# Performance work log

Measured on AMD Instinct MI355X. Metric: run time of the kernel, lower is better.

## Reference

```python
import jax, jax.numpy as jnp
import numpy as np

B, T = 16, 40
NH, DEPTH, NCLASS, IMG_H, W_IMG = 128, 2, 6625, 32, 512
HIDDEN = 64  # nh < 256 -> hidden = 64
LINEAR_IN = NH * 8  # nh * int((32-3-1)/4+1)
BN_EPS = 1e-5


def _conv2d(x, w, b, stride, pad, groups=1):
    y = jax.lax.conv_general_dilated(
        x, w, (stride, stride), [(pad, pad), (pad, pad)],
        dimension_numbers=('NCHW', 'OIHW', 'NCHW'), feature_group_count=groups)
    return y + b[None, :, None, None]


def _conv_bn_act(x, w, b, g, bb, m, v, stride, pad, groups=1):
    y = _conv2d(x, w, b, stride, pad, groups)
    y = (y - m[None, :, None, None]) * jax.lax.rsqrt(v[None, :, None, None] + BN_EPS) \
        * g[None, :, None, None] + bb[None, :, None, None]
    return jax.nn.gelu(y, approximate=False)  # torch nn.GELU default = exact erf


def _gru(xs, wih, whh, bih, bhh):
    # torch GRU gate order: r, z, n. xs: [B, T, D] -> ys: [B, T, H]
    H = whh.shape[1]
    xp = jnp.einsum('btd,gd->btg', xs, wih) + bih  # [B,T,3H]

    def step(h, xt):
        hp = h @ whh.T + bhh
        r = jax.nn.sigmoid(xt[:, :H] + hp[:, :H])
        z = jax.nn.sigmoid(xt[:, H:2 * H] + hp[:, H:2 * H])
        n = jnp.tanh(xt[:, 2 * H:] + r * hp[:, 2 * H:])
        hn = (1.0 - z) * n + z * h
        return hn, hn

    h0 = jnp.zeros((xs.shape[0], H), xs.dtype)
    _, ys = jax.lax.scan(step, h0, jnp.swapaxes(xp, 0, 1))
    return jnp.swapaxes(ys, 0, 1)


def _forward(x, targets,
             conv0_w, conv0_b, bn0_g, bn0_b, bn0_m, bn0_v,
             blk_dw_w, blk_dw_b, blk_bn1_g, blk_bn1_b, blk_bn1_m, blk_bn1_v,
             blk_pw_w, blk_pw_b, blk_bn2_g, blk_bn2_b, blk_bn2_m, blk_bn2_v,
             enc_wih, enc_whh, enc_bih, enc_bhh,
             dec_wih, dec_whh, dec_bih, dec_bhh,
             emb, q_w, q_b, k_w, k_b, e_w, e_b, fc_w, fc_b):
    h = _conv_bn_act(x, conv0_w, conv0_b, bn0_g, bn0_b, bn0_m, bn0_v, 4, 0)  # [B,NH,8,128]
    # NOTE: original code applies each MicroBlock to the SAME x (feat = block(x)); faithful here.
    feat = h
    for i in range(DEPTH):
        t = h + _conv_bn_act(h, blk_dw_w[i], blk_dw_b[i], blk_bn1_g[i], blk_bn1_b[i],
                             blk_bn1_m[i], blk_bn1_v[i], 1, 1, groups=NH)
        feat = _conv_bn_act(t, blk_pw_w[i], blk_pw_b[i], blk_bn2_g[i], blk_bn2_b[i],
                            blk_bn2_m[i], blk_bn2_v[i], 1, 0)
    Bq, C, Hf, Wf = feat.shape
    feat_v = feat.reshape(Bq, C * Hf, Wf)  # Flatten(1,2)
    # adaptive_avg_pool1d target = W/4 == Wf -> identity
    feat_v = jnp.transpose(feat_v, (0, 2, 1))  # [B, Wf, C*Hf]
    enc = _gru(feat_v, enc_wih, enc_whh, enc_bih, enc_bhh)  # [B,Wf,H]
    out_enc = enc[:, -1:, :]  # [B,1,H]
    tgt = emb[targets]  # [B,T,H]
    in_dec = jnp.concatenate([out_enc, tgt], axis=1)  # [B,T+1,H]
    y = _gru(in_dec, dec_wih, dec_whh, dec_bih, dec_bhh)  # [B,T+1,H]
    q = y @ q_w.T + q_b  # [B,Td,NH]
    k = _conv2d(feat, k_w, k_b, 1, 1)  # [B,NH,h,w]
    t2 = jnp.tanh(k[:, None] + q[:, :, :, None, None])  # [B,Td,NH,h,w]
    e = jnp.einsum('btchw,c->bthw', t2, e_w[0]) + e_b[0]  # conv1x1_2: Linear(NH,1)
    a = jax.nn.softmax(e.reshape(Bq, e.shape[1], -1), axis=-1).reshape(e.shape)
    attn_feat = jnp.einsum('bchw,bthw->btc', feat, a)  # [B,Td,NH]
    # dropout: eval mode -> identity
    return attn_feat @ fc_w.T + fc_b  # [B,Td,NCLASS]


def setup_inputs() -> dict:
    key = jax.random.key(0)
    ks = iter(jax.random.split(key, 64))

    def rn(shape, s=0.05):
        return jax.random.normal(next(ks), shape, jnp.float32) * s

    inp = {
        'x': jax.random.normal(next(ks), (B, 3, IMG_H, W_IMG), jnp.float32),
        'targets': jax.random.randint(next(ks), (B, T), 0, NCLASS),
        'conv0_w': rn((NH, 3, 4, 4)), 'conv0_b': rn((NH,)),
        'bn0_g': jnp.ones((NH,)), 'bn0_b': jnp.zeros((NH,)),
        'bn0_m': jnp.zeros((NH,)), 'bn0_v': jnp.ones((NH,)),
        'blk_dw_w': rn((DEPTH, NH, 1, 3, 3)), 'blk_dw_b': rn((DEPTH, NH)),
        'blk_bn1_g': jnp.ones((DEPTH, NH)), 'blk_bn1_b': jnp.zeros((DEPTH, NH)),
        'blk_bn1_m': jnp.zeros((DEPTH, NH)), 'blk_bn1_v': jnp.ones((DEPTH, NH)),
        'blk_pw_w': rn((DEPTH, NH, NH, 1, 1)), 'blk_pw_b': rn((DEPTH, NH)),
        'blk_bn2_g': jnp.ones((DEPTH, NH)), 'blk_bn2_b': jnp.zeros((DEPTH, NH)),
        'blk_bn2_m': jnp.zeros((DEPTH, NH)), 'blk_bn2_v': jnp.ones((DEPTH, NH)),
        'enc_wih': rn((3 * HIDDEN, LINEAR_IN)), 'enc_whh': rn((3 * HIDDEN, HIDDEN)),
        'enc_bih': jnp.zeros((3 * HIDDEN,)), 'enc_bhh': jnp.zeros((3 * HIDDEN,)),
        'dec_wih': rn((3 * HIDDEN, HIDDEN)), 'dec_whh': rn((3 * HIDDEN, HIDDEN)),
        'dec_bih': jnp.zeros((3 * HIDDEN,)), 'dec_bhh': jnp.zeros((3 * HIDDEN,)),
        'emb': rn((NCLASS, HIDDEN)).at[1].set(0.0),  # padding_idx=1
        'q_w': rn((NH, HIDDEN)), 'q_b': jnp.zeros((NH,)),
        'k_w': rn((NH, NH, 3, 3)), 'k_b': jnp.zeros((NH,)),
        'e_w': rn((1, NH)), 'e_b': jnp.zeros((1,)),
        'fc_w': rn((NCLASS, NH)), 'fc_b': jnp.zeros((NCLASS,)),
    }
    return inp


def reference(x, targets,
              conv0_w, conv0_b, bn0_g, bn0_b, bn0_m, bn0_v,
              blk_dw_w, blk_dw_b, blk_bn1_g, blk_bn1_b, blk_bn1_m, blk_bn1_v,
              blk_pw_w, blk_pw_b, blk_bn2_g, blk_bn2_b, blk_bn2_m, blk_bn2_v,
              enc_wih, enc_whh, enc_bih, enc_bhh,
              dec_wih, dec_whh, dec_bih, dec_bhh,
              emb, q_w, q_b, k_w, k_b, e_w, e_b, fc_w, fc_b):
    return _forward(x, targets,
                    conv0_w, conv0_b, bn0_g, bn0_b, bn0_m, bn0_v,
                    blk_dw_w, blk_dw_b, blk_bn1_g, blk_bn1_b, blk_bn1_m, blk_bn1_v,
                    blk_pw_w, blk_pw_b, blk_bn2_g, blk_bn2_b, blk_bn2_m, blk_bn2_v,
                    enc_wih, enc_whh, enc_bih, enc_bhh,
                    dec_wih, dec_whh, dec_bih, dec_bhh,
                    emb, q_w, q_b, k_w, k_b, e_w, e_b, fc_w, fc_b)
```

## Files before the change

### kernel.cpp

```cpp
#include <hip/hip_runtime.h>
#include <hip/hip_bf16.h>

#define DEV __device__ __forceinline__

#define B_    16
#define T_    40
#define TDEC  41
#define NH    128
#define HF    8
#define WF    128
#define HID   64
#define G3    192
#define NCLS  6625
#define SPAT  1024
#define NFRAG 415

typedef _Float16 half8 __attribute__((ext_vector_type(8)));
typedef _Float16 half2_ __attribute__((ext_vector_type(2)));
typedef float    f32x4 __attribute__((ext_vector_type(4)));
typedef float    f32x2 __attribute__((ext_vector_type(2)));

#if __has_builtin(__builtin_amdgcn_fdot2)
#define FDOT2(w,h,acc) __builtin_amdgcn_fdot2((w),(h),(acc),false)
#else
#define FDOT2(w,h,acc) ((acc) + (float)((w)[0])*(float)((h)[0]) + (float)((w)[1])*(float)((h)[1]))
#endif

DEV float sigmoidf_(float x){ return 1.0f/(1.0f + __expf(-x)); }
DEV float tanhf_(float x){ float e = __expf(2.0f*x); return 1.0f - 2.0f/(e + 1.0f); }
DEV float gelu_(float x){ return 0.5f*x*(1.0f + erff(x*0.70710678118654752f)); }
DEV float bnf_(float x, float g, float b, float m, float v){
  return (x - m)*rsqrtf(v + 1e-5f)*g + b;
}

#define SCAN_LOOP(STEPS, WRITE_ALL)                                            \
  for (int t = 0; t < (STEPS); ++t){                                           \
    float x0c = 0.f, x1c = 0.f, x2c = 0.f;                                     \
    if (t + 2 < (STEPS)){                                                      \
      const float* p = xpb + (t + 2)*G3 + g;                                   \
      x0c = p[0]; x1c = p[HID]; x2c = p[2*HID];                                \
    }                                                                          \
    const uint4* h4 = (const uint4*)hsh16;                                     \
    float a0 = b0, a1 = b1, a2 = b2;                                           \
    float d0 = 0.f, d1 = 0.f, d2 = 0.f;                                        \
    _Pragma("unroll")                                                          \
    for (int i = 0; i < 8; i += 2){                                            \
      uint4 hvA = h4[i], hvB = h4[i+1];                                        \
      DO4(hvA, i,   a0, a1, a2)                                                \
      DO4(hvB, i+1, d0, d1, d2)                                                \
    }                                                                          \
    float hp0 = a0 + d0;                                                       \
    float hp1 = a1 + d1;                                                       \
    float hp2 = a2 + d2;                                                       \
    float e0 = __expf(-(x0a + hp0));                                           \
    float r  = __builtin_amdgcn_rcpf(1.0f + e0);                               \
    float e1 = __expf(-(x1a + hp1));                                           \
    float z  = __builtin_amdgcn_rcpf(1.0f + e1);                               \
    float ag = x2a + r*hp2;                                                    \
    float ex = __expf(2.0f*ag);                                                \
    float n  = 1.0f - 2.0f*__builtin_amdgcn_rcpf(ex + 1.0f);                   \
    hg = z*(hg - n) + n;                                                       \
    if (WRITE_ALL) outp[(b*TDEC + t)*HID + g] = hg;                            \
    hsh16[g] = (_Float16)hg;                                                   \
    x0a = x0b; x1a = x1b; x2a = x2b;                                           \
    x0b = x0c; x1b = x1c; x2b = x2c;                                           \
  }

#define DO4(hv, wq, aa, bb, cc)                                                \
  { half2_ h0 = __builtin_bit_cast(half2_, hv.x);                              \
    half2_ h1 = __builtin_bit_cast(half2_, hv.y);                              \
    half2_ h2 = __builtin_bit_cast(half2_, hv.z);                              \
    half2_ h3 = __builtin_bit_cast(half2_, hv.w);                              \
    aa = FDOT2(__builtin_bit_cast(half2_, w0q[wq].x), h0, aa);                 \
    bb = FDOT2(__builtin_bit_cast(half2_, w1q[wq].x), h0, bb);                 \
    cc = FDOT2(__builtin_bit_cast(half2_, w2q[wq].x), h0, cc);                 \
    aa = FDOT2(__builtin_bit_cast(half2_, w0q[wq].y), h1, aa);                 \
    bb = FDOT2(__builtin_bit_cast(half2_, w1q[wq].y), h1, bb);                 \
    cc = FDOT2(__builtin_bit_cast(half2_, w2q[wq].y), h1, cc);                 \
    aa = FDOT2(__builtin_bit_cast(half2_, w0q[wq].z), h2, aa);                 \
    bb = FDOT2(__builtin_bit_cast(half2_, w1q[wq].z), h2, bb);                 \
    cc = FDOT2(__builtin_bit_cast(half2_, w2q[wq].z), h2, cc);                 \
    aa = FDOT2(__builtin_bit_cast(half2_, w0q[wq].w), h3, aa);                 \
    bb = FDOT2(__builtin_bit_cast(half2_, w1q[wq].w), h3, bb);                 \
    cc = FDOT2(__builtin_bit_cast(half2_, w2q[wq].w), h3, cc); }

__global__ __launch_bounds__(256) void k_conv0(const float* __restrict__ x,
    const float* __restrict__ w, const float* __restrict__ bias,
    const float* __restrict__ bng, const float* __restrict__ bnb,
    const float* __restrict__ bnm, const float* __restrict__ bnv,
    float* __restrict__ h)
{
  int tid = blockIdx.x*256 + threadIdx.x;
  int ow = tid & 127;
  int oh = (tid >> 7) & 7;
  int c4 = (tid >> 10) & 31;
  int b  = tid >> 15;
  float acc[4] = {0.f,0.f,0.f,0.f};
  int xbase = ((b*3)*32 + oh*4)*512 + ow*4;
  for (int ci = 0; ci < 3; ++ci){
    #pragma unroll
    for (int kh = 0; kh < 4; ++kh){
      float4 xv = *(const float4*)(x + xbase + ci*(32*512) + kh*512);
      #pragma unroll
      for (int cc = 0; cc < 4; ++cc){
        int co = c4*4 + cc;
        const float* wp = w + ((co*3 + ci)*4 + kh)*4;
        acc[cc] += xv.x*wp[0] + xv.y*wp[1] + xv.z*wp[2] + xv.w*wp[3];
      }
    }
  }
  #pragma unroll
  for (int cc = 0; cc < 4; ++cc){
    int co = c4*4 + cc;
    float v = acc[cc] + bias[co];
    v = bnf_(v, bng[co], bnb[co], bnm[co], bnv[co]);
    h[((b*NH + co)*HF + oh)*WF + ow] = gelu_(v);
  }
}

__global__ __launch_bounds__(256) void k_dw(const float* __restrict__ h,
    const float* __restrict__ dww, const float* __restrict__ dwb,
    const float* __restrict__ g1, const float* __restrict__ b1,
    const float* __restrict__ m1, const float* __restrict__ v1,
    float* __restrict__ t)
{
  int tid = blockIdx.x*256 + threadIdx.x;
  int ow = tid & 127;
  int oh = (tid >> 7) & 7;
  int c  = (tid >> 10) & 127;
  int b  = tid >> 17;
  const float* wp = dww + NH*9 + c*9;
  const float* hp = h + ((b*NH + c)*HF)*WF;
  float acc = 0.f;
  #pragma unroll
  for (int kh = 0; kh < 3; ++kh){
    int ih = oh + kh - 1;
    if (ih < 0 || ih >= HF) continue;
    #pragma unroll
    for (int kw = 0; kw < 3; ++kw){
      int iw = ow + kw - 1;
      if (iw < 0 || iw >= WF) continue;
      acc += hp[ih*WF + iw]*wp[kh*3 + kw];
    }
  }
  float val = acc + dwb[NH + c];
  val = bnf_(val, g1[NH + c], b1[NH + c], m1[NH + c], v1[NH + c]);
  t[tid] = hp[oh*WF + ow] + gelu_(val);
}

__global__ __launch_bounds__(256) void k_fcprep(const float* __restrict__ fcw,
    _Float16* __restrict__ fcwH, _Float16* __restrict__ fcwL)
{
  int tid = blockIdx.x*256 + threadIdx.x;
  if (tid >= NFRAG*4*64*8) return;
  int j  = tid & 7;
  int l  = (tid >> 3) & 63;
  int kf = (tid >> 9) & 3;
  int nf = tid >> 11;
  int n = nf*16 + (l & 15);
  int k = kf*32 + ((l >> 4) << 3) + j;
  float v = (n < NCLS) ? fcw[n*NH + k] : 0.f;
  _Float16 hi = (_Float16)v;
  fcwH[tid] = hi;
  fcwL[tid] = (_Float16)(v - (float)hi);
}

__global__ __launch_bounds__(256) void k_misc(const float* __restrict__ pw,
    float* __restrict__ pwT, const float* __restrict__ kw,
    _Float16* __restrict__ kwA, const int* __restrict__ tgt,
    const float* __restrict__ emb, float* __restrict__ indec,
    const float* __restrict__ encwhh, unsigned* __restrict__ enc16,
    const float* __restrict__ decwhh, unsigned* __restrict__ dec16,
    const float* __restrict__ wih, _Float16* __restrict__ wihH,
    _Float16* __restrict__ wihL)
{
  int bid = blockIdx.x;
  if (bid < 64){
    int tid = bid*256 + threadIdx.x;
    int ci = tid & 127; int co = tid >> 7;
    pwT[ci*128 + co] = pw[16384 + co*128 + ci];
  } else if (bid < 640){
    int tid = (bid - 64)*256 + threadIdx.x;
    int j = tid & 7;
    int l = (tid >> 3) & 63;
    int f = (tid >> 9) & 7;
    int s = tid >> 12;
    int co = f*16 + (l & 15);
    int k  = s*32 + ((l >> 4) << 3) + j;
    int r  = k >> 7;
    int ci = k & 127;
    kwA[tid] = (_Float16)kw[(co*128 + ci)*9 + r];
  } else if (bid < 800){
    int tid = (bid - 640)*256 + threadIdx.x;
    if (tid >= B_*T_*HID) return;
    int j = tid & 63; int rest = tid >> 6;
    int t = rest % T_; int b = rest / T_;
    int cls = tgt[b*T_ + t];
    indec[(b*TDEC + 1 + t)*HID + j] = emb[cls*HID + j];
  } else if (bid < 848){
    int seg = bid - 800;
    const float* src = (seg < 24) ? encwhh : decwhh;
    unsigned* dst    = (seg < 24) ? enc16   : dec16;
    int tid = (seg % 24)*256 + threadIdx.x;
    int r = tid >> 5; int k2 = tid & 31;
    half2_ hv;
    hv[0] = (_Float16)src[r*HID + 2*k2];
    hv[1] = (_Float16)src[r*HID + 2*k2 + 1];
    dst[tid] = __builtin_bit_cast(unsigned, hv);
  } else {
    int tid = (bid - 848)*256 + threadIdx.x;
    if (tid >= 12*32*64*8) return;
    int j  = tid & 7;
    int l  = (tid >> 3) & 63;
    int kf = (tid >> 9) & 31;
    int nf = tid >> 14;
    int n = nf*16 + (l & 15);
    int k = kf*32 + ((l >> 4) << 3) + j;
    float v = wih[n*1024 + k];
    _Float16 hi = (_Float16)v;
    wihH[tid] = hi;
    wihL[tid] = (_Float16)(v - (float)hi);
  }
}

__global__ __launch_bounds__(512) void k_pw(const float* __restrict__ t,
    const float* __restrict__ pwT, const float* __restrict__ pwb,
    const float* __restrict__ g2, const float* __restrict__ b2,
    const float* __restrict__ m2, const float* __restrict__ v2,
    float* __restrict__ feat)
{
  int bid = blockIdx.x;
  int wh = bid & 1; int oh = (bid >> 1) & 7; int b = bid >> 4;
  int w0 = wh*64;
  int tid = threadIdx.x;
  __shared__ __align__(16) float tile[128*64];
  for (int i = 0; i < 16; ++i){
    int e = i*512 + tid; int ci = e >> 6; int wloc = e & 63;
    tile[ci*64 + wloc] = t[((b*NH + ci)*HF + oh)*WF + w0 + wloc];
  }
  __syncthreads();
  int co = tid & 127; int wq = tid >> 7;
  float acc[16];
  #pragma unroll
  for (int i = 0; i < 16; ++i) acc[i] = 0.f;
  for (int ci = 0; ci < 128; ++ci){
    float wt = pwT[ci*128 + co];
    const float4* tp = (const float4*)(tile + ci*64 + wq*16);
    #pragma unroll
    for (int j = 0; j < 4; ++j){
      float4 tv = tp[j];
      acc[j*4+0] += tv.x*wt; acc[j*4+1] += tv.y*wt;
      acc[j*4+2] += tv.z*wt; acc[j*4+3] += tv.w*wt;
    }
  }
  float bb = pwb[128 + co];
  float gg = g2[128 + co], bc = b2[128 + co], mm = m2[128 + co], vv = v2[128 + co];
  float* op = feat + ((b*NH + co)*HF + oh)*WF + w0 + wq*16;
  #pragma unroll
  for (int i = 0; i < 16; ++i){
    float v = bnf_(acc[i] + bb, gg, bc, mm, vv);
    op[i] = gelu_(v);
  }
}

__global__ __launch_bounds__(64) void k_encxp3(const float* __restrict__ feat,
    const uint4* __restrict__ wihH, const uint4* __restrict__ wihL,
    const float* __restrict__ bih, float* __restrict__ xp)
{
  int bid = blockIdx.x;
  int mf = bid & 127;
  int ny = bid >> 7;
  int l  = threadIdx.x;
  int b  = mf >> 3, wc = mf & 7;
  int m_w = wc*16 + (l & 15);
  f32x4 acc0{0.f,0.f,0.f,0.f}, acc1{0.f,0.f,0.f,0.f}, acc2{0.f,0.f,0.f,0.f};
  int nf0 = ny*3;
  for (int kf = 0; kf < 32; ++kf){
    int ci = kf*4 + (l >> 4);
    const float* ap = feat + ((b*NH + ci)*HF)*WF + m_w;
    float av[8];
    #pragma unroll
    for (int j = 0; j < 8; ++j) av[j] = ap[j*WF];
    half8 ah, al;
    #pragma unroll
    for (int j = 0; j < 8; ++j){
      ah[j] = (_Float16)av[j];
      al[j] = (_Float16)(av[j] - (float)ah[j]);
    }
    uint4 bH0 = wihH[((nf0+0)*32 + kf)*64 + l];
    uint4 bL0 = wihL[((nf0+0)*32 + kf)*64 + l];
    uint4 bH1 = wihH[((nf0+1)*32 + kf)*64 + l];
    uint4 bL1 = wihL[((nf0+1)*32 + kf)*64 + l];
    uint4 bH2 = wihH[((nf0+2)*32 + kf)*64 + l];
    uint4 bL2 = wihL[((nf0+2)*32 + kf)*64 + l];
    #define ACCUM(accv, bH, bL) {                                              \
      half8 wh = __builtin_bit_cast(half8, bH);                                \
      half8 wl = __builtin_bit_cast(half8, bL);                                \
      accv = __builtin_amdgcn_mfma_f32_16x16x32_f16(ah, wh, accv, 0, 0, 0);    \
      accv = __builtin_amdgcn_mfma_f32_16x16x32_f16(al, wh, accv, 0, 0, 0);    \
      accv = __builtin_amdgcn_mfma_f32_16x16x32_f16(ah, wl, accv, 0, 0, 0);    \
    }
    ACCUM(acc0, bH0, bL0)
    ACCUM(acc1, bH1, bL1)
    ACCUM(acc2, bH2, bL2)
    #undef ACCUM
  }
  int mbase = b*WF + wc*16 + ((l >> 4) << 2);
  #pragma unroll
  for (int i = 0; i < 3; ++i){
    f32x4 a = (i == 0) ? acc0 : (i == 1) ? acc1 : acc2;
    int n = (nf0 + i)*16 + (l & 15);
    float bias = bih[n];
    #pragma unroll
    for (int q = 0; q < 4; ++q)
      xp[(mbase + q)*G3 + n] = a[q] + bias;
  }
}

template<int STEPS, bool WRITE_ALL>
__global__ __attribute__((amdgpu_waves_per_eu(1, 1))) __launch_bounds__(64)
void k_scan2(const float* __restrict__ xp, const uint4* __restrict__ whh16,
             const float* __restrict__ bhh, float* __restrict__ outp)
{
  __shared__ __align__(16) _Float16 hsh16[HID];
  int g = threadIdx.x;
  int b = blockIdx.x;
  uint4 w0q[8], w1q[8], w2q[8];
  const uint4* q0 = whh16 + g*8;
  const uint4* q1 = whh16 + (HID + g)*8;
  const uint4* q2 = whh16 + (2*HID + g)*8;
  #pragma unroll
  for (int k = 0; k < 8; ++k){ w0q[k] = q0[k]; w1q[k] = q1[k]; w2q[k] = q2[k]; }
  float b0 = bhh[g], b1 = bhh[HID + g], b2 = bhh[2*HID + g];
  float hg = 0.f;
  hsh16[g] = (_Float16)0.f;
  const float* xpb = xp + b*STEPS*G3;
  float x0a = xpb[g], x1a = xpb[HID + g], x2a = xpb[2*HID + g];
  float x0b = 0.f, x1b = 0.f, x2b = 0.f;
  if (STEPS > 1){
    const float* p = xpb + G3 + g;
    x0b = p[0]; x1b = p[HID]; x2b = p[2*HID];
  }
  SCAN_LOOP(STEPS, WRITE_ALL)
  if (!WRITE_ALL) outp[(b*TDEC)*HID + g] = hg;
}

__global__ __launch_bounds__(64) void k_escan_conv(
    const float* __restrict__ xp, const uint4* __restrict__ whh16,
    const float* __restrict__ bhh, float* __restrict__ outp,
    const float* __restrict__ feat, const uint4* __restrict__ kwA4,
    const float* __restrict__ kb, float* __restrict__ ko)
{
  __shared__ __align__(16) _Float16 hsh16[HID];
  int bigid = blockIdx.x;
  if (bigid < 16){
    __builtin_amdgcn_s_setprio(3);
    int g = threadIdx.x;
    int b = bigid;
    uint4 w0q[8], w1q[8], w2q[8];
    const uint4* q0 = whh16 + g*8;
    const uint4* q1 = whh16 + (HID + g)*8;
    const uint4* q2 = whh16 + (2*HID + g)*8;
    #pragma unroll
    for (int k = 0; k < 8; ++k){ w0q[k] = q0[k]; w1q[k] = q1[k]; w2q[k] = q2[k]; }
    float b0 = bhh[g], b1 = bhh[HID + g], b2 = bhh[2*HID + g];
    float hg = 0.f;
    hsh16[g] = (_Float16)0.f;
    const float* xpb = xp + b*WF*G3;
    float x0a = xpb[g], x1a = xpb[HID + g], x2a = xpb[2*HID + g];
    float x0b = 0.f, x1b = 0.f, x2b = 0.f;
    {
      const float* p = xpb + G3 + g;
      x0b = p[0]; x1b = p[HID]; x2b = p[2*HID];
    }
    SCAN_LOOP(WF, false)
    outp[(b*TDEC)*HID + g] = hg;
    __builtin_amdgcn_s_setprio(0);
    return;
  }
  int bid = bigid - 16;
  int b  = ((bid & 7) << 1) | ((bid >> 3) & 1);
  int mq = (bid >> 4) & 3;
  int cs = (bid >> 6) & 3;
  int wq = (bid >> 8) & 1;
  int oh = (bid >> 9) & 7;
  int l  = threadIdx.x;
  int w0 = wq*64 + mq*16;
  int iwb = w0 + (l & 15);
  int cib = (l >> 4) << 3;

  f32x4 acc0{0.f,0.f,0.f,0.f}, acc1{0.f,0.f,0.f,0.f};
  uint4 a0A, a0B, a1A, a1B;
  float b0v[8], b1v[8];

  #define ISS(s, aX, aY, bvv) {                                               \
    aX = kwA4[(s)*512 + cs*128 + l];                                          \
    aY = kwA4[(s)*512 + cs*128 + 64 + l];                                     \
    int r = (s) >> 2; int dh = r/3 - 1; int dw2 = r%3 - 1;                    \
    int ci0 = ((s) & 3) << 5;                                                 \
    int ih = oh + dh; int iw = iwb + dw2;                                     \
    bool ok = (ih >= 0) & (ih < HF) & (iw >= 0) & (iw < WF);                  \
    const float* fp = feat + ((b*NH + ci0 + cib)*HF + ih)*WF + iw;            \
    _Pragma("unroll")                                                         \
    for (int jj = 0; jj < 8; ++jj) bvv[jj] = ok ? fp[jj*(HF*WF)] : 0.f;       \
  }
  #define CMP(aX, aY, bvv) {                                                  \
    half8 bf;                                                                 \
    _Pragma("unroll")                                                         \
    for (int jj = 0; jj < 8; ++jj) bf[jj] = (_Float16)bvv[jj];                \
    half8 af0 = __builtin_bit_cast(half8, aX);                                \
    half8 af1 = __builtin_bit_cast(half8, aY);                                \
    acc0 = __builtin_amdgcn_mfma_f32_16x16x32_f16(af0, bf, acc0, 0, 0, 0);    \
    acc1 = __builtin_amdgcn_mfma_f32_16x16x32_f16(af1, bf, acc1, 0, 0, 0);    \
  }

  ISS(0, a0A, a0B, b0v);
  for (int s = 0; s < 36; s += 2){
    if (s + 1 < 36) ISS(s + 1, a1A, a1B, b1v);
    CMP(a0A, a0B, b0v);
    if (s + 2 < 36) ISS(s + 2, a0A, a0B, b0v);
    if (s + 1 < 36) CMP(a1A, a1B, b1v);
  }
  #undef ISS
  #undef CMP

  int m = w0 + (l & 15);
  #pragma unroll
  for (int q = 0; q < 4; ++q){
    int co0 = cs*32 + ((l >> 4) << 2) + q;
    int co1 = co0 + 16;
    ko[((b*NH + co0)*HF + oh)*WF + m] = acc0[q] + kb[co0];
    ko[((b*NH + co1)*HF + oh)*WF + m] = acc1[q] + kb[co1];
  }
}

__global__ void k_xpd(const float* __restrict__ indec, const float* __restrict__ wih,
                      const float* __restrict__ bih, float* __restrict__ xpd)
{
  int tid = blockIdx.x*256 + threadIdx.x;
  if (tid >= B_*TDEC*G3) return;
  int g = tid % G3; int bt = tid / G3;
  const float4* r4 = (const float4*)(indec + bt*HID);
  const float4* w4 = (const float4*)(wih + g*HID);
  float acc = bih[g];
  #pragma unroll
  for (int j = 0; j < 16; ++j){
    float4 rv = r4[j], wv = w4[j];
    acc += rv.x*wv.x + rv.y*wv.y + rv.z*wv.z + rv.w*wv.w;
  }
  xpd[tid] = acc;
}

__global__ void k_q(const float* __restrict__ y, const float* __restrict__ qw,
                    const float* __restrict__ qb0, float* __restrict__ q)
{
  int tid = blockIdx.x*256 + threadIdx.x;
  if (tid >= B_*TDEC*NH) return;
  int co = tid & 127; int bt = tid >> 7;
  const float4* r4 = (const float4*)(y + bt*HID);
  const float4* w4 = (const float4*)(qw + co*HID);
  float acc = qb0[co];
  #pragma unroll
  for (int j = 0; j < 16; ++j){
    float4 rv = r4[j], wv = w4[j];
    acc += rv.x*wv.x + rv.y*wv.y + rv.z*wv.z + rv.w*wv.w;
  }
  q[tid] = acc;
}

__global__ __launch_bounds__(512) void k_e3(const float* __restrict__ k,
    const float* __restrict__ q, const float* __restrict__ ew,
    const float* __restrict__ eb, float* __restrict__ e)
{
  int bid = blockIdx.x;
  int st = bid & 15; int b = bid >> 4;
  int s0 = st*64;
  int tid = threadIdx.x;
  __shared__ float ksh[NH*64];
  __shared__ float qsh[TDEC*NH];
  __shared__ float ewsh[NH];
  #pragma unroll
  for (int i = 0; i < 16; ++i){
    int e2 = i*512 + tid; int c = e2 >> 6; int j = e2 & 63;
    ksh[e2] = k[(b*NH + c)*SPAT + s0 + j];
  }
  #pragma unroll
  for (int i = 0; i < 11; ++i){
    int e2 = i*512 + tid;
    if (e2 < TDEC*NH) qsh[e2] = q[b*TDEC*NH + e2];
  }
  if (tid < NH) ewsh[tid] = ew[tid];
  __syncthreads();
  int sl = tid & 63; int tp = tid >> 6;
  float ebv = eb[0];
  float acc[6] = {ebv, ebv, ebv, ebv, ebv, ebv};
  #pragma unroll 2
  for (int c = 0; c < NH; ++c){
    float kv = ksh[c*64 + sl];
    float ewc = ewsh[c];
    #pragma unroll
    for (int i = 0; i < 6; ++i){
      int t = tp + i*8;
      if (t < TDEC){
        float v = kv + qsh[t*NH + c];
        float ex = __expf(2.0f*v);
        float rc = __builtin_amdgcn_rcpf(ex + 1.0f);
        acc[i] += ewc*(1.0f - 2.0f*rc);
      }
    }
  }
  #pragma unroll
  for (int i = 0; i < 6; ++i){
    int t = tp + i*8;
    if (t < TDEC) e[(b*TDEC + t)*SPAT + s0 + sl] = acc[i];
  }
}

__global__ __launch_bounds__(256) void k_attnf2(const float* __restrict__ feat,
    const float* __restrict__ e, float* __restrict__ attnf)
{
  int bid = blockIdx.x;
  int ch = bid & 1; int rest = bid >> 1;
  int tq = rest % 11; int b = rest / 11;
  int tid = threadIdx.x;
  __shared__ __align__(16) float ash[4*SPAT];
  __shared__ float psh[4*4*64];
  __shared__ float sinv[4];
  for (int i = 0; i < 16; ++i){
    int e2 = i*256 + tid; int tt = e2 >> 10; int s = e2 & 1023;
    int t = tq*4 + tt;
    ash[e2] = (t < TDEC) ? e[(b*TDEC + t)*SPAT + s] : 0.f;
  }
  __syncthreads();
  {
    int w = tid >> 6; int l = tid & 63;
    float* row = ash + w*SPAT;
    float vreg[16];
    float mx = -1e30f;
    #pragma unroll
    for (int j = 0; j < 16; ++j){ vreg[j] = row[l + j*64]; mx = fmaxf(mx, vreg[j]); }
    #pragma unroll
    for (int m = 1; m < 64; m <<= 1) mx = fmaxf(mx, __shfl_xor(mx, m));
    float sum = 0.f;
    #pragma unroll
    for (int j = 0; j < 16; ++j){
      float ev = __expf(vreg[j] - mx);
      row[l + j*64] = ev;
      sum += ev;
    }
    #pragma unroll
    for (int m = 1; m < 64; m <<= 1) sum += __shfl_xor(sum, m);
    if (l == 0) sinv[w] = 1.0f/sum;
  }
  __syncthreads();
  int cl = tid & 63; int sq = tid >> 6;
  const float* fp = feat + (b*NH + ch*64 + cl)*SPAT + sq*256;
  float acc[4] = {0.f,0.f,0.f,0.f};
  for (int i = 0; i < 64; ++i){
    float4 fv = *(const float4*)(fp + i*4);
    #pragma unroll
    for (int tt = 0; tt < 4; ++tt){
      const float* ar = ash + tt*SPAT + sq*256 + i*4;
      acc[tt] += fv.x*ar[0] + fv.y*ar[1] + fv.z*ar[2] + fv.w*ar[3];
    }
  }
  #pragma unroll
  for (int tt = 0; tt < 4; ++tt) psh[(sq*4 + tt)*64 + cl] = acc[tt];
  __syncthreads();
  {
    int tt = tid >> 6; int c2 = tid & 63;
    int t = tq*4 + tt;
    if (t < TDEC){
      float v = psh[(0*4 + tt)*64 + c2] + psh[(1*4 + tt)*64 + c2]
              + psh[(2*4 + tt)*64 + c2] + psh[(3*4 + tt)*64 + c2];
      attnf[(b*TDEC + t)*NH + ch*64 + c2] = v*sinv[tt];
    }
  }
}

__global__ __launch_bounds__(256) void k_fc2(const float* __restrict__ attnf,
    const uint4* __restrict__ fcwH, const uint4* __restrict__ fcwL,
    const float* __restrict__ fcb, float* __restrict__ out)
{
  int mf = blockIdx.x;
  int ny = blockIdx.y;
  int tid = threadIdx.x;
  int l = tid & 63, w = tid >> 6;
  half8 ah[4], al[4];
  const float* ap = attnf + (mf*16 + (l & 15))*NH + ((l >> 4) << 3);
  #pragma unroll
  for (int kf = 0; kf < 4; ++kf){
    float4 v0 = *(const float4*)(ap + kf*32);
    float4 v1 = *(const float4*)(ap + kf*32 + 4);
    float vv[8] = {v0.x, v0.y, v0.z, v0.w, v1.x, v1.y, v1.z, v1.w};
    half8 h, lo;
    #pragma unroll
    for (int j = 0; j < 8; ++j){
      h[j]  = (_Float16)vv[j];
      lo[j] = (_Float16)(vv[j] - (float)h[j]);
    }
    ah[kf] = h; al[kf] = lo;
  }
  #pragma unroll
  for (int i = 0; i < 4; ++i){
    int nf = ny*16 + w*4 + i;
    if (nf >= NFRAG) return;
    f32x4 acc{0.f,0.f,0.f,0.f};
    #pragma unroll
    for (int kf = 0; kf < 4; ++kf){
      uint4 bH = fcwH[(nf*4 + kf)*64 + l];
      uint4 bL = fcwL[(nf*4 + kf)*64 + l];
      half8 wh = __builtin_bit_cast(half8, bH);
      half8 wl = __builtin_bit_cast(half8, bL);
      acc = __builtin_amdgcn_mfma_f32_16x16x32_f16(ah[kf], wh, acc, 0, 0, 0);
      acc = __builtin_amdgcn_mfma_f32_16x16x32_f16(al[kf], wh, acc, 0, 0, 0);
      acc = __builtin_amdgcn_mfma_f32_16x16x32_f16(ah[kf], wl, acc, 0, 0, 0);
    }
    int n = nf*16 + (l & 15);
    if (n < NCLS){
      float bias = fcb[n];
      int mrow = mf*16 + ((l >> 4) << 2);
      #pragma unroll
      for (int q = 0; q < 4; ++q)
        out[(mrow + q)*NCLS + n] = acc[q] + bias;
    }
  }
}

extern "C" void kernel_launch(void* const* d_in, const int* in_sizes, int n_in,
                              void* d_out, int out_size, void* d_ws, size_t ws_size,
                              hipStream_t stream)
{
  (void)in_sizes; (void)n_in; (void)out_size; (void)ws_size;
  const float* x      = (const float*)d_in[0];
  const int*   tgt    = (const int*)  d_in[1];
  const float* conv0w = (const float*)d_in[2];
  const float* conv0b = (const float*)d_in[3];
  const float* bn0g   = (const float*)d_in[4];
  const float* bn0b   = (const float*)d_in[5];
  const float* bn0m   = (const float*)d_in[6];
  const float* bn0v   = (const float*)d_in[7];
  const float* dww    = (const float*)d_in[8];
  const float* dwb    = (const float*)d_in[9];
  const float* bn1g   = (const float*)d_in[10];
  const float* bn1b   = (const float*)d_in[11];
  const float* bn1m   = (const float*)d_in[12];
  const float* bn1v   = (const float*)d_in[13];
  const float* pww    = (const float*)d_in[14];
  const float* pwb    = (const float*)d_in[15];
  const float* bn2g   = (const float*)d_in[16];
  const float* bn2b   = (const float*)d_in[17];
  const float* bn2m   = (const float*)d_in[18];
  const float* bn2v   = (const float*)d_in[19];
  const float* encwih = (const float*)d_in[20];
  const float* encwhh = (const float*)d_in[21];
  const float* encbih = (const float*)d_in[22];
  const float* encbhh = (const float*)d_in[23];
  const float* decwih = (const float*)d_in[24];
  const float* decwhh = (const float*)d_in[25];
  const float* decbih = (const float*)d_in[26];
  const float* decbhh = (const float*)d_in[27];
  const float* emb    = (const float*)d_in[28];
  const float* qw     = (const float*)d_in[29];
  const float* qb0    = (const float*)d_in[30];
  const float* kw     = (const float*)d_in[31];
  const float* kb     = (const float*)d_in[32];
  const float* ew     = (const float*)d_in[33];
  const float* eb     = (const float*)d_in[34];
  const float* fcw    = (const float*)d_in[35];
  const float* fcb    = (const float*)d_in[36];

  float* ws    = (float*)d_ws;
  float* hbuf  = ws + 0;
  float* tbuf  = ws + 2097152;
  float* feat  = ws + 4194304;
  float* xp    = ws + 6291456;
  float* indec = ws + 6684672;
  float* xpd   = ws + 6726656;
  float* ybuf  = ws + 6852608;
  float* qbuf  = ws + 6894592;
  float* attf  = ws + 6978560;
  float* pwT   = ws + 7062528;
  _Float16* kwA = (_Float16*)(ws + 7078912);
  unsigned* enc16 = (unsigned*)(ws + 7152640);
  unsigned* dec16 = (unsigned*)(ws + 7158784);
  _Float16* fcwH = (_Float16*)(ws + 7164928);
  _Float16* fcwL = (_Float16*)(ws + 7589888);
  _Float16* wihH = (_Float16*)(ws + 6726656);
  _Float16* wihL = (_Float16*)(ws + 6852608);
  float* kbuf  = hbuf;
  float* ebuf  = tbuf;
  float* out   = (float*)d_out;

  hipLaunchKernelGGL(k_conv0,   dim3(2048),        dim3(256), 0, stream,
                     x, conv0w, conv0b, bn0g, bn0b, bn0m, bn0v, hbuf);
  hipLaunchKernelGGL(k_dw,      dim3(8192),        dim3(256), 0, stream,
                     hbuf, dww, dwb, bn1g, bn1b, bn1m, bn1v, tbuf);
  hipLaunchKernelGGL(k_misc,    dim3(1616),        dim3(256), 0, stream,
                     pww, pwT, kw, kwA, tgt, emb, indec,
                     encwhh, enc16, decwhh, dec16, encwih, wihH, wihL);
  hipLaunchKernelGGL(k_fcprep,  dim3(3320),        dim3(256), 0, stream,
                     fcw, fcwH, fcwL);
  hipLaunchKernelGGL(k_pw,      dim3(256),         dim3(512), 0, stream,
                     tbuf, pwT, pwb, bn2g, bn2b, bn2m, bn2v, feat);
  hipLaunchKernelGGL(k_encxp3,  dim3(512),         dim3(64), 0, stream,
                     feat, (const uint4*)wihH, (const uint4*)wihL, encbih, xp);
  hipLaunchKernelGGL(k_escan_conv, dim3(4112),     dim3(64), 0, stream,
                     xp, (const uint4*)enc16, encbhh, indec,
                     feat, (const uint4*)kwA, kb, kbuf);
  hipLaunchKernelGGL(k_xpd,     dim3(492),         dim3(256), 0, stream,
                     indec, decwih, decbih, xpd);
  hipLaunchKernelGGL((k_scan2<TDEC,true>), dim3(16), dim3(64), 0, stream,
                     xpd, (const uint4*)dec16, decbhh, ybuf);
  hipLaunchKernelGGL(k_q,       dim3(328),         dim3(256), 0, stream,
                     ybuf, qw, qb0, qbuf);
  hipLaunchKernelGGL(k_e3,      dim3(256),         dim3(512), 0, stream,
                     kbuf, qbuf, ew, eb, ebuf);
  hipLaunchKernelGGL(k_attnf2,  dim3(352),         dim3(256), 0, stream,
                     feat, ebuf, attf);
  hipLaunchKernelGGL(k_fc2,     dim3(41, 26),      dim3(256), 0, stream,
                     attf, (const uint4*)fcwH, (const uint4*)fcwL, fcb, out);
}
```

Measured before the change: 260.3 us.

## Fuse prep kernels into front kernel; pre-transpose feat to fp16 channel-last for conv

Merges conv0, the misc weight-prep kernel and the fc weight-prep kernel into one launch, which removes two kernel launches. Adds a kernel that converts feat to fp16 in a [b, spatial, channel] layout, so the 3x3 key-conv MFMA loop fetches each B fragment with one 16-byte load. Before, it made eight strided fp32 gathers and converted each value. This costs an extra launch and a transpose pass over feat, with the fp16 buffer placed inside the tbuf workspace region.

Measured after the change: 272.1 us. +4.5%, slower.

```diff
diff --git a/kernel.cpp b/kernel.cpp
--- a/kernel.cpp
+++ b/kernel.cpp
@@ -84,37 +84,111 @@
     bb = FDOT2(__builtin_bit_cast(half2_, w1q[wq].w), h3, bb);                 \
     cc = FDOT2(__builtin_bit_cast(half2_, w2q[wq].w), h3, cc); }
 
-__global__ __launch_bounds__(256) void k_conv0(const float* __restrict__ x,
-    const float* __restrict__ w, const float* __restrict__ bias,
-    const float* __restrict__ bng, const float* __restrict__ bnb,
-    const float* __restrict__ bnm, const float* __restrict__ bnv,
-    float* __restrict__ h)
-{
-  int tid = blockIdx.x*256 + threadIdx.x;
-  int ow = tid & 127;
-  int oh = (tid >> 7) & 7;
-  int c4 = (tid >> 10) & 31;
-  int b  = tid >> 15;
-  float acc[4] = {0.f,0.f,0.f,0.f};
-  int xbase = ((b*3)*32 + oh*4)*512 + ow*4;
-  for (int ci = 0; ci < 3; ++ci){
-    #pragma unroll
-    for (int kh = 0; kh < 4; ++kh){
-      float4 xv = *(const float4*)(x + xbase + ci*(32*512) + kh*512);
+__global__ __launch_bounds__(256) void k_front(
+    const float* __restrict__ x, const float* __restrict__ w,
+    const float* __restrict__ bias, const float* __restrict__ bng,
+    const float* __restrict__ bnb, const float* __restrict__ bnm,
+    const float* __restrict__ bnv, float* __restrict__ h,
+    const float* __restrict__ pw, float* __restrict__ pwT,
+    const float* __restrict__ kw, _Float16* __restrict__ kwA,
+    const int* __restrict__ tgt, const float* __restrict__ emb,
+    float* __restrict__ indec,
+    const float* __restrict__ encwhh, unsigned* __restrict__ enc16,
+    const float* __restrict__ decwhh, unsigned* __restrict__ dec16,
+    const float* __restrict__ wih, _Float16* __restrict__ wihH,
+    _Float16* __restrict__ wihL,
+    const float* __restrict__ fcw, _Float16* __restrict__ fcwH,
+    _Float16* __restrict__ fcwL)
+{
+  int bid = blockIdx.x;
+  if (bid < 2048){
+    int tid = bid*256 + threadIdx.x;
+    int ow = tid & 127;
+    int oh = (tid >> 7) & 7;
+    int c4 = (tid >> 10) & 31;
+    int b  = tid >> 15;
+    float acc[4] = {0.f,0.f,0.f,0.f};
+    int xbase = ((b*3)*32 + oh*4)*512 + ow*4;
+    for (int ci = 0; ci < 3; ++ci){
       #pragma unroll
-      for (int cc = 0; cc < 4; ++cc){
-        int co = c4*4 + cc;
-        const float* wp = w + ((co*3 + ci)*4 + kh)*4;
-        acc[cc] += xv.x*wp[0] + xv.y*wp[1] + xv.z*wp[2] + xv.w*wp[3];
+      for (int kh = 0; kh < 4; ++kh){
+        float4 xv = *(const float4*)(x + xbase + ci*(32*512) + kh*512);
+        #pragma unroll
+        for (int cc = 0; cc < 4; ++cc){
+          int co = c4*4 + cc;
+          const float* wp = w + ((co*3 + ci)*4 + kh)*4;
+          acc[cc] += xv.x*wp[0] + xv.y*wp[1] + xv.z*wp[2] + xv.w*wp[3];
+        }
       }
     }
-  }
-  #pragma unroll
-  for (int cc = 0; cc < 4; ++cc){
-    int co = c4*4 + cc;
-    float v = acc[cc] + bias[co];
-    v = bnf_(v, bng[co], bnb[co], bnm[co], bnv[co]);
-    h[((b*NH + co)*HF + oh)*WF + ow] = gelu_(v);
+    #pragma unroll
+    for (int cc = 0; cc < 4; ++cc){
+      int co = c4*4 + cc;
+      float v = acc[cc] + bias[co];
+      v = bnf_(v, bng[co], bnb[co], bnm[co], bnv[co]);
+      h[((b*NH + co)*HF + oh)*WF + ow] = gelu_(v);
+    }
+  } else if (bid < 3664){
+    int mbid = bid - 2048;
+    if (mbid < 64){
+      int tid = mbid*256 + threadIdx.x;
+      int ci = tid & 127; int co = tid >> 7;
+      pwT[ci*128 + co] = pw[16384 + co*128 + ci];
+    } else if (mbid < 640){
+      int tid = (mbid - 64)*256 + threadIdx.x;
+      int j = tid & 7;
+      int l = (tid >> 3) & 63;
+      int f = (tid >> 9) & 7;
+      int s = tid >> 12;
+      int co = f*16 + (l & 15);
+      int k  = s*32 + ((l >> 4) << 3) + j;
+      int r  = k >> 7;
+      int ci = k & 127;
+      kwA[tid] = (_Float16)kw[(co*128 + ci)*9 + r];
+    } else if (mbid < 800){
+      int tid = (mbid - 640)*256 + threadIdx.x;
+      if (tid >= B_*T_*HID) return;
+      int j = tid & 63; int rest = tid >> 6;
+      int t = rest % T_; int b = rest / T_;
+      int cls = tgt[b*T_ + t];
+      indec[(b*TDEC + 1 + t)*HID + j] = emb[cls*HID + j];
+    } else if (mbid < 848){
+      int seg = mbid - 800;
+      const float* src = (seg < 24) ? encwhh : decwhh;
+      unsigned* dst    = (seg < 24) ? enc16   : dec16;
+      int tid = (seg % 24)*256 + threadIdx.x;
+      int r = tid >> 5; int k2 = tid & 31;
+      half2_ hv;
+      hv[0] = (_Float16)src[r*HID + 2*k2];
+      hv[1] = (_Float16)src[r*HID + 2*k2 + 1];
+      dst[tid] = __builtin_bit_cast(unsigned, hv);
+    } else {
+      int tid = (mbid - 848)*256 + threadIdx.x;
+      if (tid >= 12*32*64*8) return;
+      int j  = tid & 7;
+      int l  = (tid >> 3) & 63;
+      int kf = (tid >> 9) & 31;
+      int nf = tid >> 14;
+      int n = nf*16 + (l & 15);
+      int k = kf*32 + ((l >> 4) << 3) + j;
+      float v = wih[n*1024 + k];
+      _Float16 hi = (_Float16)v;
+      wihH[tid] = hi;
+      wihL[tid] = (_Float16)(v - (float)hi);
+    }
+  } else {
+    int tid = (bid - 3664)*256 + threadIdx.x;
+    if (tid >= NFRAG*4*64*8) return;
+    int j  = tid & 7;
+    int l  = (tid >> 3) & 63;
+    int kf = (tid >> 9) & 3;
+    int nf = tid >> 11;
+    int n = nf*16 + (l & 15);
+    int k = kf*32 + ((l >> 4) << 3) + j;
+    float v = (n < NCLS) ? fcw[n*NH + k] : 0.f;
+    _Float16 hi = (_Float16)v;
+    fcwH[tid] = hi;
+    fcwL[tid] = (_Float16)(v - (float)hi);
   }
 }
 
@@ -148,81 +222,6 @@
   t[tid] = hp[oh*WF + ow] + gelu_(val);
 }
 
-__global__ __launch_bounds__(256) void k_fcprep(const float* __restrict__ fcw,
-    _Float16* __restrict__ fcwH, _Float16* __restrict__ fcwL)
-{
-  int tid = blockIdx.x*256 + threadIdx.x;
-  if (tid >= NFRAG*4*64*8) return;
-  int j  = tid & 7;
-  int l  = (tid >> 3) & 63;
-  int kf = (tid >> 9) & 3;
-  int nf = tid >> 11;
-  int n = nf*16 + (l & 15);
-  int k = kf*32 + ((l >> 4) << 3) + j;
-  float v = (n < NCLS) ? fcw[n*NH + k] : 0.f;
-  _Float16 hi = (_Float16)v;
-  fcwH[tid] = hi;
-  fcwL[tid] = (_Float16)(v - (float)hi);
-}
-
-__global__ __launch_bounds__(256) void k_misc(const float* __restrict__ pw,
-    float* __restrict__ pwT, const float* __restrict__ kw,
-    _Float16* __restrict__ kwA, const int* __restrict__ tgt,
-    const float* __restrict__ emb, float* __restrict__ indec,
-    const float* __restrict__ encwhh, unsigned* __restrict__ enc16,
-    const float* __restrict__ decwhh, unsigned* __restrict__ dec16,
-    const float* __restrict__ wih, _Float16* __restrict__ wihH,
-    _Float16* __restrict__ wihL)
-{
-  int bid = blockIdx.x;
-  if (bid < 64){
-    int tid = bid*256 + threadIdx.x;
-    int ci = tid & 127; int co = tid >> 7;
-    pwT[ci*128 + co] = pw[16384 + co*128 + ci];
-  } else if (bid < 640){
-    int tid = (bid - 64)*256 + threadIdx.x;
-    int j = tid & 7;
-    int l = (tid >> 3) & 63;
-    int f = (tid >> 9) & 7;
-    int s = tid >> 12;
-    int co = f*16 + (l & 15);
-    int k  = s*32 + ((l >> 4) << 3) + j;
-    int r  = k >> 7;
-    int ci = k & 127;
-    kwA[tid] = (_Float16)kw[(co*128 + ci)*9 + r];
-  } else if (bid < 800){
-    int tid = (bid - 640)*256 + threadIdx.x;
-    if (tid >= B_*T_*HID) return;
-    int j = tid & 63; int rest = tid >> 6;
-    int t = rest % T_; int b = rest / T_;
-    int cls = tgt[b*T_ + t];
-    indec[(b*TDEC + 1 + t)*HID + j] = emb[cls*HID + j];
-  } else if (bid < 848){
-    int seg = bid - 800;
-    const float* src = (seg < 24) ? encwhh : decwhh;
-    unsigned* dst    = (seg < 24) ? enc16   : dec16;
-    int tid = (seg % 24)*256 + threadIdx.x;
-    int r = tid >> 5; int k2 = tid & 31;
-    half2_ hv;
-    hv[0] = (_Float16)src[r*HID + 2*k2];
-    hv[1] = (_Float16)src[r*HID + 2*k2 + 1];
-    dst[tid] = __builtin_bit_cast(unsigned, hv);
-  } else {
-    int tid = (bid - 848)*256 + threadIdx.x;
-    if (tid >= 12*32*64*8) return;
-    int j  = tid & 7;
-    int l  = (tid >> 3) & 63;
-    int kf = (tid >> 9) & 31;
-    int nf = tid >> 14;
-    int n = nf*16 + (l & 15);
-    int k = kf*32 + ((l >> 4) << 3) + j;
-    float v = wih[n*1024 + k];
-    _Float16 hi = (_Float16)v;
-    wihH[tid] = hi;
-    wihL[tid] = (_Float16)(v - (float)hi);
-  }
-}
-
 __global__ __launch_bounds__(512) void k_pw(const float* __restrict__ t,
     const float* __restrict__ pwT, const float* __restrict__ pwb,
     const float* __restrict__ g2, const float* __restrict__ b2,
@@ -260,6 +259,27 @@
   for (int i = 0; i < 16; ++i){
     float v = bnf_(acc[i] + bb, gg, bc, mm, vv);
     op[i] = gelu_(v);
+  }
+}
+
+__global__ __launch_bounds__(256) void k_t16(const float* __restrict__ feat,
+    _Float16* __restrict__ f16T)
+{
+  int bid = blockIdx.x;
+  int st = bid & 15; int b = bid >> 4;
+  int s0 = st*64;
+  int tid = threadIdx.x;
+  __shared__ _Float16 til[NH][66];
+  #pragma unroll
+  for (int i = 0; i < 32; ++i){
+    int e = i*256 + tid; int c = e >> 6; int j = e & 63;
+    til[c][j] = (_Float16)feat[(b*NH + c)*SPAT + s0 + j];
+  }
+  __syncthreads();
+  #pragma unroll
+  for (int i = 0; i < 32; ++i){
+    int e = i*256 + tid; int c = e & 127; int j = e >> 7;
+    f16T[(b*SPAT + s0 + j)*NH + c] = til[c][j];
   }
 }
 
@@ -348,7 +368,7 @@
 __global__ __launch_bounds__(64) void k_escan_conv(
     const float* __restrict__ xp, const uint4* __restrict__ whh16,
     const float* __restrict__ bhh, float* __restrict__ outp,
-    const float* __restrict__ feat, const uint4* __restrict__ kwA4,
+    const _Float16* __restrict__ f16T, const uint4* __restrict__ kwA4,
     const float* __restrict__ kb, float* __restrict__ ko)
 {
   __shared__ __align__(16) _Float16 hsh16[HID];
@@ -390,36 +410,32 @@
   int cib = (l >> 4) << 3;
 
   f32x4 acc0{0.f,0.f,0.f,0.f}, acc1{0.f,0.f,0.f,0.f};
-  uint4 a0A, a0B, a1A, a1B;
-  float b0v[8], b1v[8];
-
-  #define ISS(s, aX, aY, bvv) {                                               \
+  uint4 a0A, a0B, a1A, a1B, b0q, b1q;
+
+  #define ISS(s, aX, aY, bq) {                                                \
     aX = kwA4[(s)*512 + cs*128 + l];                                          \
     aY = kwA4[(s)*512 + cs*128 + 64 + l];                                     \
     int r = (s) >> 2; int dh = r/3 - 1; int dw2 = r%3 - 1;                    \
     int ci0 = ((s) & 3) << 5;                                                 \
     int ih = oh + dh; int iw = iwb + dw2;                                     \
     bool ok = (ih >= 0) & (ih < HF) & (iw >= 0) & (iw < WF);                  \
-    const float* fp = feat + ((b*NH + ci0 + cib)*HF + ih)*WF + iw;            \
-    _Pragma("unroll")                                                         \
-    for (int jj = 0; jj < 8; ++jj) bvv[jj] = ok ? fp[jj*(HF*WF)] : 0.f;       \
-  }
-  #define CMP(aX, aY, bvv) {                                                  \
-    half8 bf;                                                                 \
-    _Pragma("unroll")                                                         \
-    for (int jj = 0; jj < 8; ++jj) bf[jj] = (_Float16)bvv[jj];                \
+    bq = uint4{0u,0u,0u,0u};                                                  \
+    if (ok) bq = *(const uint4*)(f16T + (b*SPAT + ih*WF + iw)*NH + ci0 + cib);\
+  }
+  #define CMP(aX, aY, bq) {                                                   \
+    half8 bf  = __builtin_bit_cast(half8, bq);                                \
     half8 af0 = __builtin_bit_cast(half8, aX);                                \
     half8 af1 = __builtin_bit_cast(half8, aY);                                \
     acc0 = __builtin_amdgcn_mfma_f32_16x16x32_f16(af0, bf, acc0, 0, 0, 0);    \
     acc1 = __builtin_amdgcn_mfma_f32_16x16x32_f16(af1, bf, acc1, 0, 0, 0);    \
   }
 
-  ISS(0, a0A, a0B, b0v);
+  ISS(0, a0A, a0B, b0q);
   for (int s = 0; s < 36; s += 2){
-    if (s + 1 < 36) ISS(s + 1, a1A, a1B, b1v);
-    CMP(a0A, a0B, b0v);
-    if (s + 2 < 36) ISS(s + 2, a0A, a0B, b0v);
-    if (s + 1 < 36) CMP(a1A, a1B, b1v);
+    if (s + 1 < 36) ISS(s + 1, a1A, a1B, b1q);
+    CMP(a0A, a0B, b0q);
+    if (s + 2 < 36) ISS(s + 2, a0A, a0B, b0q);
+    if (s + 1 < 36) CMP(a1A, a1B, b1q);
   }
   #undef ISS
   #undef CMP
@@ -688,26 +704,27 @@
   _Float16* fcwL = (_Float16*)(ws + 7589888);
   _Float16* wihH = (_Float16*)(ws + 6726656);
   _Float16* wihL = (_Float16*)(ws + 6852608);
+  _Float16* f16T = (_Float16*)(ws + 3145728);
   float* kbuf  = hbuf;
   float* ebuf  = tbuf;
   float* out   = (float*)d_out;
 
-  hipLaunchKernelGGL(k_conv0,   dim3(2048),        dim3(256), 0, stream,
-                     x, conv0w, conv0b, bn0g, bn0b, bn0m, bn0v, hbuf);
+  hipLaunchKernelGGL(k_front,   dim3(6984),        dim3(256), 0, stream,
+                     x, conv0w, conv0b, bn0g, bn0b, bn0m, bn0v, hbuf,
+                     pww, pwT, kw, kwA, tgt, emb, indec,
+                     encwhh, enc16, decwhh, dec16, encwih, wihH, wihL,
+                     fcw, fcwH, fcwL);
   hipLaunchKernelGGL(k_dw,      dim3(8192),        dim3(256), 0, stream,
                      hbuf, dww, dwb, bn1g, bn1b, bn1m, bn1v, tbuf);
-  hipLaunchKernelGGL(k_misc,    dim3(1616),        dim3(256), 0, stream,
-                     pww, pwT, kw, kwA, tgt, emb, indec,
-                     encwhh, enc16, decwhh, dec16, encwih, wihH, wihL);
-  hipLaunchKernelGGL(k_fcprep,  dim3(3320),        dim3(256), 0, stream,
-                     fcw, fcwH, fcwL);
   hipLaunchKernelGGL(k_pw,      dim3(256),         dim3(512), 0, stream,
                      tbuf, pwT, pwb, bn2g, bn2b, bn2m, bn2v, feat);
+  hipLaunchKernelGGL(k_t16,     dim3(256),         dim3(256), 0, stream,
+                     feat, f16T);
   hipLaunchKernelGGL(k_encxp3,  dim3(512),         dim3(64), 0, stream,
                      feat, (const uint4*)wihH, (const uint4*)wihL, encbih, xp);
   hipLaunchKernelGGL(k_escan_conv, dim3(4112),     dim3(64), 0, stream,
                      xp, (const uint4*)enc16, encbhh, indec,
-                     feat, (const uint4*)kwA, kb, kbuf);
+                     f16T, (const uint4*)kwA, kb, kbuf);
   hipLaunchKernelGGL(k_xpd,     dim3(492),         dim3(256), 0, stream,
                      indec, decwih, decbih, xpd);
   hipLaunchKernelGGL((k_scan2<TDEC,true>), dim3(16), dim3(64), 0, stream,
```
